# Optimization experiments

Hardware: AMD Instinct MI355X
Metric: run time of the kernel (lower is better)

The kernel has to match this reference:

```python
import jax, jax.numpy as jnp
import numpy as np

NUM_LAYERS = 32
HIDDEN_DIM = 2048
RANK = 64
BATCH = 2048


def setup_inputs() -> dict:
    key = jax.random.key(0)
    k_z, k_id, k_u, k_v = jax.random.split(key, 4)
    z = jax.random.normal(k_z, (BATCH, HIDDEN_DIM), dtype=jnp.float32)
    layer_ids = jax.random.randint(k_id, (BATCH,), 0, NUM_LAYERS)
    u = jax.random.normal(k_u, (NUM_LAYERS, HIDDEN_DIM, RANK), dtype=jnp.float32) * 0.01
    v = jax.random.normal(k_v, (NUM_LAYERS, HIDDEN_DIM, RANK), dtype=jnp.float32) * 0.01
    return {"z": z, "layer_ids": layer_ids, "u": u, "v": v}


def reference(z, layer_ids, u, v):
    # Gather per-sample low-rank factors: [B, H, R]
    u_g = u[layer_ids]
    v_g = v[layer_ids]
    # proj = V_l^T z : [B, R]
    proj = jnp.einsum('bhr,bh->br', v_g, z)
    # delta = U_l proj : [B, H]
    delta = jnp.einsum('bhr,br->bh', u_g, proj)
    return z + delta
```

## Files before the change

### kernel.cpp

```cpp
#include <hip/hip_runtime.h>

#define NUM_LAYERS 32
#define HIDDEN 2048
#define RANK 64
#define BATCH 2048
#define CHK 256
#define SCP 4
#define MB 16
#define ZPAD 264
#define PPAD 72
#define PREPPAD 264

typedef __attribute__((ext_vector_type(8))) short bf16x8;
typedef __attribute__((ext_vector_type(4))) float f32x4;

static __device__ __forceinline__ ushort f2bf(float x) {
    unsigned b = __builtin_bit_cast(unsigned, x);
    b += 0x7fffu + ((b >> 16) & 1u);
    return (ushort)(b >> 16);
}
static __device__ __forceinline__ ushort4 pack4(float4 v) {
    ushort4 r; r.x = f2bf(v.x); r.y = f2bf(v.y); r.z = f2bf(v.z); r.w = f2bf(v.w);
    return r;
}


__global__ __launch_bounds__(256)
void k_prep(const float* __restrict__ v, const float* __restrict__ u,
            const int* __restrict__ ids,
            ushort* __restrict__ vbf, ushort* __restrict__ ubf,
            float* __restrict__ proj,
            int* __restrict__ counts, int* __restrict__ offsets,
            int* __restrict__ perm)
{
    const int b = blockIdx.x, t = threadIdx.x;
    if (b < 256) {
        const int l = b >> 3, kbase = (b & 7) * CHK;
        __shared__ ushort vtile[RANK * PREPPAD];
        #pragma unroll
        for (int it = 0; it < 16; ++it) {
            const int idx = it * 256 + t;
            const int hh = idx >> 4, rq = idx & 15;
            const float4 f = *(const float4*)
                &v[((size_t)l * HIDDEN + kbase + hh) * RANK + rq * 4];
            vtile[(rq * 4 + 0) * PREPPAD + hh] = f2bf(f.x);
            vtile[(rq * 4 + 1) * PREPPAD + hh] = f2bf(f.y);
            vtile[(rq * 4 + 2) * PREPPAD + hh] = f2bf(f.z);
            vtile[(rq * 4 + 3) * PREPPAD + hh] = f2bf(f.w);
        }
        __syncthreads();
        #pragma unroll
        for (int it = 0; it < 8; ++it) {
            const int idx = it * 256 + t;
            const int r = idx >> 5, c = idx & 31;
            const bf16x8 d = *(const bf16x8*)&vtile[r * PREPPAD + c * 8];
            *(bf16x8*)&vbf[((size_t)l * RANK + r) * HIDDEN + kbase + c * 8] = d;
        }
    } else if (b < 512) {
        const int bb = b - 256;
        const int l = bb >> 3, hbase = (bb & 7) * CHK;
        #pragma unroll
        for (int it = 0; it < 16; ++it) {
            const int idx = it * 256 + t;
            const int hh = idx >> 4, rq = idx & 15;
            const size_t off = ((size_t)l * HIDDEN + hbase + hh) * RANK + rq * 4;
            const float4 f = *(const float4*)&u[off];
            *(ushort4*)&ubf[off] = pack4(f);
        }
    } else if (b < 576) {
        const int base = (b - 512) * (BATCH * RANK / 64);
        for (int i = t; i < BATCH * RANK / 64; i += 256) proj[base + i] = 0.0f;
    } else {
        __shared__ int cnt[NUM_LAYERS];
        __shared__ int off[NUM_LAYERS];
        __shared__ int cur[NUM_LAYERS];
        if (t < NUM_LAYERS) cnt[t] = 0;
        __syncthreads();
        for (int i = t; i < BATCH; i += 256) atomicAdd(&cnt[ids[i]], 1);
        __syncthreads();
        if (t == 0) {
            int a = 0;
            for (int l = 0; l < NUM_LAYERS; ++l) { off[l] = a; a += cnt[l]; }
        }
        __syncthreads();
        if (t < NUM_LAYERS) { cur[t] = 0; counts[t] = cnt[t]; offsets[t] = off[t]; }
        __syncthreads();
        for (int i = t; i < BATCH; i += 256) {
            int l = ids[i];
            int p = off[l] + atomicAdd(&cur[l], 1);
            perm[p] = i;
        }
    }
}

__global__ __launch_bounds__(256)
void k_proj(const float* __restrict__ z, const ushort* __restrict__ vbf,
            const int* __restrict__ counts, const int* __restrict__ offsets,
            const int* __restrict__ perm, float* __restrict__ proj)
{
    const int kc = blockIdx.x, l = blockIdx.y, sc = blockIdx.z;
    const int n = counts[l], o = offsets[l];
    if (sc * MB >= n) return;
    const int t = threadIdx.x;
    const int w = t >> 6, lane = t & 63;
    const int m16 = lane & 15, quad = lane >> 4;
    const int kbase = kc * CHK;

    __shared__ ushort zt[MB * ZPAD];
    __shared__ int bidx[MB];

    const ushort* vb = vbf + ((size_t)l * RANK + w * 16 + m16) * HIDDEN
                     + kbase + quad * 8;

    for (int base = sc * MB; base < n; base += SCP * MB) {
        const int nb = (n - base < MB) ? (n - base) : MB;
        __syncthreads();
        if (t < MB) bidx[t] = (t < nb) ? perm[o + base + t] : 0;
        __syncthreads();
        #pragma unroll
        for (int it = 0; it < 4; ++it) {
            const int idx = it * 256 + t;
            const int si = idx >> 6, q = idx & 63;
            const float4 f = *(const float4*)
                &z[(size_t)bidx[si] * HIDDEN + kbase + q * 4];
            *(ushort4*)&zt[si * ZPAD + q * 4] = pack4(f);
        }
        __syncthreads();

        f32x4 acc = {0.f, 0.f, 0.f, 0.f};
        #pragma unroll
        for (int kt = 0; kt < 8; ++kt) {
            const bf16x8 a = *(const bf16x8*)&zt[m16 * ZPAD + kt * 32 + quad * 8];
            const bf16x8 bm = *(const bf16x8*)&vb[kt * 32];
            acc = __builtin_amdgcn_mfma_f32_16x16x32_bf16(a, bm, acc, 0, 0, 0);
        }
        #pragma unroll
        for (int reg = 0; reg < 4; ++reg) {
            const int row = quad * 4 + reg;
            if (row < nb)
                atomicAdd(&proj[(size_t)bidx[row] * RANK + w * 16 + m16], acc[reg]);
        }
    }
}

__global__ __launch_bounds__(256)
void k_delta(const float* __restrict__ z, const ushort* __restrict__ ubf,
             const int* __restrict__ counts, const int* __restrict__ offsets,
             const int* __restrict__ perm, const float* __restrict__ proj,
             float* __restrict__ out)
{
    const int hc = blockIdx.x, l = blockIdx.y, sc = blockIdx.z;
    const int n = counts[l], o = offsets[l];
    if (sc * MB >= n) return;
    const int t = threadIdx.x;
    const int w = t >> 6, lane = t & 63;
    const int m16 = lane & 15, quad = lane >> 4;
    const int hbase = hc * CHK;

    __shared__ ushort pt[MB * PPAD];
    __shared__ int bidx[MB];

    const ushort* ub = ubf + ((size_t)l * HIDDEN + hbase) * RANK;

    for (int base = sc * MB; base < n; base += SCP * MB) {
        const int nb = (n - base < MB) ? (n - base) : MB;
        __syncthreads();
        if (t < MB) bidx[t] = (t < nb) ? perm[o + base + t] : 0;
        __syncthreads();
        {
            const int si = t >> 4, rq = t & 15;
            const float4 f = *(const float4*)&proj[(size_t)bidx[si] * RANK + rq * 4];
            *(ushort4*)&pt[si * PPAD + rq * 4] = pack4(f);
        }
        __syncthreads();

        const bf16x8 pa0 = *(const bf16x8*)&pt[m16 * PPAD + quad * 8];
        const bf16x8 pa1 = *(const bf16x8*)&pt[m16 * PPAD + 32 + quad * 8];

        f32x4 acc[4];
        #pragma unroll
        for (int nt = 0; nt < 4; ++nt) acc[nt] = (f32x4){0.f, 0.f, 0.f, 0.f};
        #pragma unroll
        for (int nt = 0; nt < 4; ++nt) {
            const int hcol = (w * 4 + nt) * 16 + m16;
            const bf16x8 b0 = *(const bf16x8*)&ub[hcol * RANK + quad * 8];
            const bf16x8 b1 = *(const bf16x8*)&ub[hcol * RANK + 32 + quad * 8];
            acc[nt] = __builtin_amdgcn_mfma_f32_16x16x32_bf16(pa0, b0, acc[nt], 0, 0, 0);
            acc[nt] = __builtin_amdgcn_mfma_f32_16x16x32_bf16(pa1, b1, acc[nt], 0, 0, 0);
        }
        #pragma unroll
        for (int reg = 0; reg < 4; ++reg) {
            const int si = quad * 4 + reg;
            if (si < nb) {
                const size_t rowb = (size_t)bidx[si] * HIDDEN + hbase;
                #pragma unroll
                for (int nt = 0; nt < 4; ++nt) {
                    const int hcol = (w * 4 + nt) * 16 + m16;
                    out[rowb + hcol] = z[rowb + hcol] + acc[nt][reg];
                }
            }
        }
    }
}

extern "C" void kernel_launch(void* const* d_in, const int* in_sizes, int n_in,
                              void* d_out, int out_size, void* d_ws, size_t ws_size,
                              hipStream_t stream)
{
    const float* z   = (const float*)d_in[0];
    const int*   ids = (const int*)d_in[1];
    const float* u   = (const float*)d_in[2];
    const float* v   = (const float*)d_in[3];
    float* out = (float*)d_out;

    ushort* vbf  = (ushort*)d_ws;
    ushort* ubf  = vbf + (size_t)NUM_LAYERS * RANK * HIDDEN;
    float*  proj = (float*)(ubf + (size_t)NUM_LAYERS * HIDDEN * RANK);
    int* counts  = (int*)(proj + (size_t)BATCH * RANK);
    int* offsets = counts + NUM_LAYERS;
    int* perm    = offsets + NUM_LAYERS;

    hipLaunchKernelGGL(k_prep, dim3(577), dim3(256), 0, stream,
                       v, u, ids, vbf, ubf, proj, counts, offsets, perm);
    hipLaunchKernelGGL(k_proj, dim3(HIDDEN / CHK, NUM_LAYERS, SCP), dim3(256), 0, stream,
                       z, vbf, counts, offsets, perm, proj);
    hipLaunchKernelGGL(k_delta, dim3(HIDDEN / CHK, NUM_LAYERS, SCP), dim3(256), 0, stream,
                       z, ubf, counts, offsets, perm, proj, out);
}
```

Measured before the change: 114.9 us.

## Drop weight pre-conversion pass and convert fp32 factors to bf16 in-register

Removes the prep stage that transposed V and converted U/V to bf16 in workspace; k_proj and k_delta now load fp32 factors directly and convert them in registers before the MFMA. k_proj also stops staging z through LDS and loads each lane's z row directly, removing a barrier. This saves writing and re-reading the converted weight copies. In exchange, it doubles the bytes of weight reads, makes the V reads strided and poorly coalesced, and repeats the conversion for each sample chunk.

```diff
diff --git a/kernel.cpp b/kernel.cpp
--- a/kernel.cpp
+++ b/kernel.cpp
@@ -7,9 +7,7 @@
 #define CHK 256
 #define SCP 4
 #define MB 16
-#define ZPAD 264
 #define PPAD 72
-#define PREPPAD 264
 
 typedef __attribute__((ext_vector_type(8))) short bf16x8;
 typedef __attribute__((ext_vector_type(4))) float f32x4;
@@ -23,54 +21,23 @@
     ushort4 r; r.x = f2bf(v.x); r.y = f2bf(v.y); r.z = f2bf(v.z); r.w = f2bf(v.w);
     return r;
 }
+static __device__ __forceinline__ bf16x8 cvt8(float4 a, float4 b) {
+    bf16x8 r;
+    r[0] = (short)f2bf(a.x); r[1] = (short)f2bf(a.y);
+    r[2] = (short)f2bf(a.z); r[3] = (short)f2bf(a.w);
+    r[4] = (short)f2bf(b.x); r[5] = (short)f2bf(b.y);
+    r[6] = (short)f2bf(b.z); r[7] = (short)f2bf(b.w);
+    return r;
+}
 
 
 __global__ __launch_bounds__(256)
-void k_prep(const float* __restrict__ v, const float* __restrict__ u,
-            const int* __restrict__ ids,
-            ushort* __restrict__ vbf, ushort* __restrict__ ubf,
-            float* __restrict__ proj,
-            int* __restrict__ counts, int* __restrict__ offsets,
-            int* __restrict__ perm)
+void k_setup(const int* __restrict__ ids, float* __restrict__ proj,
+             int* __restrict__ counts, int* __restrict__ offsets,
+             int* __restrict__ perm)
 {
-    const int b = blockIdx.x, t = threadIdx.x;
-    if (b < 256) {
-        const int l = b >> 3, kbase = (b & 7) * CHK;
-        __shared__ ushort vtile[RANK * PREPPAD];
-        #pragma unroll
-        for (int it = 0; it < 16; ++it) {
-            const int idx = it * 256 + t;
-            const int hh = idx >> 4, rq = idx & 15;
-            const float4 f = *(const float4*)
-                &v[((size_t)l * HIDDEN + kbase + hh) * RANK + rq * 4];
-            vtile[(rq * 4 + 0) * PREPPAD + hh] = f2bf(f.x);
-            vtile[(rq * 4 + 1) * PREPPAD + hh] = f2bf(f.y);
-            vtile[(rq * 4 + 2) * PREPPAD + hh] = f2bf(f.z);
-            vtile[(rq * 4 + 3) * PREPPAD + hh] = f2bf(f.w);
-        }
-        __syncthreads();
-        #pragma unroll
-        for (int it = 0; it < 8; ++it) {
-            const int idx = it * 256 + t;
-            const int r = idx >> 5, c = idx & 31;
-            const bf16x8 d = *(const bf16x8*)&vtile[r * PREPPAD + c * 8];
-            *(bf16x8*)&vbf[((size_t)l * RANK + r) * HIDDEN + kbase + c * 8] = d;
-        }
-    } else if (b < 512) {
-        const int bb = b - 256;
-        const int l = bb >> 3, hbase = (bb & 7) * CHK;
-        #pragma unroll
-        for (int it = 0; it < 16; ++it) {
-            const int idx = it * 256 + t;
-            const int hh = idx >> 4, rq = idx & 15;
-            const size_t off = ((size_t)l * HIDDEN + hbase + hh) * RANK + rq * 4;
-            const float4 f = *(const float4*)&u[off];
-            *(ushort4*)&ubf[off] = pack4(f);
-        }
-    } else if (b < 576) {
-        const int base = (b - 512) * (BATCH * RANK / 64);
-        for (int i = t; i < BATCH * RANK / 64; i += 256) proj[base + i] = 0.0f;
-    } else {
+    const int t = threadIdx.x;
+    if (blockIdx.x == 0) {
         __shared__ int cnt[NUM_LAYERS];
         __shared__ int off[NUM_LAYERS];
         __shared__ int cur[NUM_LAYERS];
@@ -90,11 +57,14 @@
             int p = off[l] + atomicAdd(&cur[l], 1);
             perm[p] = i;
         }
+    } else {
+        const int base = (blockIdx.x - 1) * (BATCH * RANK / 64);
+        for (int i = t; i < BATCH * RANK / 64; i += 256) proj[base + i] = 0.0f;
     }
 }
 
 __global__ __launch_bounds__(256)
-void k_proj(const float* __restrict__ z, const ushort* __restrict__ vbf,
+void k_proj(const float* __restrict__ z, const float* __restrict__ v,
             const int* __restrict__ counts, const int* __restrict__ offsets,
             const int* __restrict__ perm, float* __restrict__ proj)
 {
@@ -106,32 +76,30 @@
     const int m16 = lane & 15, quad = lane >> 4;
     const int kbase = kc * CHK;
 
-    __shared__ ushort zt[MB * ZPAD];
     __shared__ int bidx[MB];
 
-    const ushort* vb = vbf + ((size_t)l * RANK + w * 16 + m16) * HIDDEN
-                     + kbase + quad * 8;
+    const float* vp = v + ((size_t)l * HIDDEN + kbase + quad * 8) * RANK
+                    + w * 16 + m16;
 
     for (int base = sc * MB; base < n; base += SCP * MB) {
         const int nb = (n - base < MB) ? (n - base) : MB;
         __syncthreads();
         if (t < MB) bidx[t] = (t < nb) ? perm[o + base + t] : 0;
         __syncthreads();
-        #pragma unroll
-        for (int it = 0; it < 4; ++it) {
-            const int idx = it * 256 + t;
-            const int si = idx >> 6, q = idx & 63;
-            const float4 f = *(const float4*)
-                &z[(size_t)bidx[si] * HIDDEN + kbase + q * 4];
-            *(ushort4*)&zt[si * ZPAD + q * 4] = pack4(f);
-        }
-        __syncthreads();
+
+        const float* zp = z + (size_t)bidx[m16] * HIDDEN + kbase + quad * 8;
 
         f32x4 acc = {0.f, 0.f, 0.f, 0.f};
         #pragma unroll
         for (int kt = 0; kt < 8; ++kt) {
-            const bf16x8 a = *(const bf16x8*)&zt[m16 * ZPAD + kt * 32 + quad * 8];
-            const bf16x8 bm = *(const bf16x8*)&vb[kt * 32];
+            const float4 a0 = *(const float4*)&zp[kt * 32];
+            const float4 a1 = *(const float4*)&zp[kt * 32 + 4];
+            float vj[8];
+            #pragma unroll
+            for (int j = 0; j < 8; ++j) vj[j] = vp[(size_t)(kt * 32 + j) * RANK];
+            const bf16x8 a  = cvt8(a0, a1);
+            const bf16x8 bm = cvt8(make_float4(vj[0], vj[1], vj[2], vj[3]),
+                                   make_float4(vj[4], vj[5], vj[6], vj[7]));
             acc = __builtin_amdgcn_mfma_f32_16x16x32_bf16(a, bm, acc, 0, 0, 0);
         }
         #pragma unroll
@@ -144,7 +112,7 @@
 }
 
 __global__ __launch_bounds__(256)
-void k_delta(const float* __restrict__ z, const ushort* __restrict__ ubf,
+void k_delta(const float* __restrict__ z, const float* __restrict__ u,
              const int* __restrict__ counts, const int* __restrict__ offsets,
              const int* __restrict__ perm, const float* __restrict__ proj,
              float* __restrict__ out)
@@ -160,7 +128,7 @@
     __shared__ ushort pt[MB * PPAD];
     __shared__ int bidx[MB];
 
-    const ushort* ub = ubf + ((size_t)l * HIDDEN + hbase) * RANK;
+    const float* ub = u + ((size_t)l * HIDDEN + hbase) * RANK;
 
     for (int base = sc * MB; base < n; base += SCP * MB) {
         const int nb = (n - base < MB) ? (n - base) : MB;
@@ -183,8 +151,11 @@
         #pragma unroll
         for (int nt = 0; nt < 4; ++nt) {
             const int hcol = (w * 4 + nt) * 16 + m16;
-            const bf16x8 b0 = *(const bf16x8*)&ub[hcol * RANK + quad * 8];
-            const bf16x8 b1 = *(const bf16x8*)&ub[hcol * RANK + 32 + quad * 8];
+            const float* ur = ub + (size_t)hcol * RANK;
+            const bf16x8 b0 = cvt8(*(const float4*)&ur[quad * 8],
+                                   *(const float4*)&ur[quad * 8 + 4]);
+            const bf16x8 b1 = cvt8(*(const float4*)&ur[32 + quad * 8],
+                                   *(const float4*)&ur[32 + quad * 8 + 4]);
             acc[nt] = __builtin_amdgcn_mfma_f32_16x16x32_bf16(pa0, b0, acc[nt], 0, 0, 0);
             acc[nt] = __builtin_amdgcn_mfma_f32_16x16x32_bf16(pa1, b1, acc[nt], 0, 0, 0);
         }
@@ -213,17 +184,15 @@
     const float* v   = (const float*)d_in[3];
     float* out = (float*)d_out;
 
-    ushort* vbf  = (ushort*)d_ws;
-    ushort* ubf  = vbf + (size_t)NUM_LAYERS * RANK * HIDDEN;
-    float*  proj = (float*)(ubf + (size_t)NUM_LAYERS * HIDDEN * RANK);
+    float* proj  = (float*)d_ws;
     int* counts  = (int*)(proj + (size_t)BATCH * RANK);
     int* offsets = counts + NUM_LAYERS;
     int* perm    = offsets + NUM_LAYERS;
 
-    hipLaunchKernelGGL(k_prep, dim3(577), dim3(256), 0, stream,
-                       v, u, ids, vbf, ubf, proj, counts, offsets, perm);
+    hipLaunchKernelGGL(k_setup, dim3(65), dim3(256), 0, stream,
+                       ids, proj, counts, offsets, perm);
     hipLaunchKernelGGL(k_proj, dim3(HIDDEN / CHK, NUM_LAYERS, SCP), dim3(256), 0, stream,
-                       z, vbf, counts, offsets, perm, proj);
+                       z, v, counts, offsets, perm, proj);
     hipLaunchKernelGGL(k_delta, dim3(HIDDEN / CHK, NUM_LAYERS, SCP), dim3(256), 0, stream,
-                       z, ubf, counts, offsets, perm, proj, out);
+                       z, u, counts, offsets, perm, proj, out);
 }
```

After: 116.6 us. Within noise of the previous version (+1.5%).
